# Kernel optimization log

Measured on AMD Instinct MI355X. Metric: run time of the kernel, lower is better.

The kernel has to match this reference:

```python
import jax, jax.numpy as jnp
import numpy as np
import math

B, N, D = 2, 4096, 1024
H, R, M = 16, 4, 8
BUCKET = 64

def setup_inputs() -> dict:
    key = jax.random.key(0)
    k1, k2, k3, k4, k5 = jax.random.split(key, 5)
    d = D // H
    return {
        "query": jax.random.normal(k1, (B, N, D), jnp.float32),
        "key": jax.random.normal(k2, (B, N, D), jnp.float32),
        "value": jax.random.normal(k3, (B, N, D), jnp.float32),
        "valence": jax.random.uniform(k4, (B,), jnp.float32),
        "hash_projections": jax.random.normal(k5, (R, H, d, M), jnp.float32),
        "valence_scale": jnp.ones((1,), jnp.float32),
    }

def reference(query, key, value, valence, hash_projections, valence_scale):
    b, n, dm = query.shape
    h = H
    d = dm // h
    r, _, _, m = hash_projections.shape
    c = n // BUCKET  # n_buckets (must divide exactly, matching torch view)
    # (B,N,D) -> (B,H,N,d)
    Q = query.reshape(b, n, h, d).transpose(0, 2, 1, 3)
    K = key.reshape(b, n, h, d).transpose(0, 2, 1, 3)
    V = value.reshape(b, n, h, d).transpose(0, 2, 1, 3)
    # LSH hash: argmax over M random projections per round -> (B,R,H,N)
    hashes = jnp.einsum('bhnd,rhdm->brhnm', Q, hash_projections)
    codes = jnp.argmax(hashes, axis=-1)
    # valence modulation (torch: scale.long().clamp(1, M); int truncation)
    scale = 1.0 + valence_scale[0] * valence.mean()
    scale_i = jnp.clip(scale.astype(jnp.int32), 1, m)
    codes = codes * scale_i
    # sort positions by hash code per (B,R,H)
    idx = jnp.argsort(codes, axis=-1)  # (B,R,H,N)
    idx_e = idx[..., None]  # (B,R,H,N,1), broadcasts over d
    K_sorted = jnp.take_along_axis(K[:, None], idx_e, axis=3)  # (B,R,H,N,d)
    V_sorted = jnp.take_along_axis(V[:, None], idx_e, axis=3)
    Kb = K_sorted.reshape(b, r, h, c, BUCKET, d)
    Vb = V_sorted.reshape(b, r, h, c, BUCKET, d)
    # NOTE: queries are bucketed in ORIGINAL order (faithful to source)
    Qb = Q.reshape(b, h, c, BUCKET, d)
    scores = jnp.einsum('bhcsd,brhced->brhcse', Qb, Kb) / math.sqrt(d)
    attn = jax.nn.softmax(scores, axis=-1)  # (B,R,H,C,S,E)
    outb = jnp.einsum('brhcse,brhced->brhcsd', attn, Vb)
    out = outb.reshape(b, r, h, n, d).mean(axis=1)  # average over hash rounds
    out = out.transpose(0, 2, 1, 3).reshape(b, n, dm)  # dropout is identity (eval)
    return out, attn.mean(axis=(1, 2))
```

## Files before the change

kernel.cpp:

```cpp
#include <hip/hip_runtime.h>
#include <hip/hip_bf16.h>

#define BB 2
#define NN 4096
#define DD 1024
#define HH 16
#define RR 4
#define MM 8
#define CC 64
#define DH 64
#define PAD 68

typedef __attribute__((ext_vector_type(8))) short bf16x8;
typedef __attribute__((ext_vector_type(4))) float f32x4;
typedef unsigned long long u64;

__device__ __forceinline__ unsigned short f2bf(float x) {
  union { __hip_bfloat16 b; unsigned short u; } cv;
  cv.b = __float2bfloat16(x);
  return cv.u;
}
__device__ __forceinline__ int swz(int row, int colbyte) {
  return row * 128 + (colbyte ^ ((row & 7) << 4));
}
__device__ __forceinline__ bf16x8 pack8(float4 a, float4 b, float sc) {
  bf16x8 r;
  const float* pa = (const float*)&a;
  const float* pb = (const float*)&b;
#pragma unroll
  for (int j = 0; j < 4; ++j) {
    r[j] = (short)f2bf(pa[j] * sc);
    r[j + 4] = (short)f2bf(pb[j] * sc);
  }
  return r;
}
__device__ __forceinline__ void load_lds16(const void* g, void* l) {
  __builtin_amdgcn_global_load_lds(
      (const __attribute__((address_space(1))) unsigned*)g,
      (__attribute__((address_space(3))) unsigned*)l, 16, 0, 0);
}

__global__ __launch_bounds__(256) void k_hash(const float* __restrict__ q,
                                              const float* __restrict__ proj,
                                              int* __restrict__ codes) {
  int blk = blockIdx.x;
  int nc = blk & (CC - 1);
  int h = (blk >> 6) & (HH - 1);
  int b = blk >> 10;
  __shared__ float Qs[64][PAD];
  __shared__ float Ps[DH][MM];
  __shared__ float Ss[64][9];
  int tid = threadIdx.x;
  const float* qbase = q + ((size_t)(b * NN + nc * 64) * DD + h * DH);
  for (int f = tid; f < 1024; f += 256) {
    int row = f >> 4, c4 = f & 15;
    *(float4*)&Qs[row][c4 * 4] = *(const float4*)(qbase + (size_t)row * DD + c4 * 4);
  }
  int nl = tid >> 3, m = tid & 7;
  for (int r = 0; r < RR; ++r) {
    const float* pbase = proj + (size_t)(r * HH + h) * DH * MM;
    for (int f = tid; f < DH * MM / 4; f += 256)
      ((float4*)Ps)[f] = ((const float4*)pbase)[f];
    __syncthreads();
    float s0 = 0.f, s1 = 0.f;
#pragma unroll
    for (int kk = 0; kk < DH; ++kk) {
      float p = Ps[kk][m];
      s0 += Qs[nl][kk] * p;
      s1 += Qs[nl + 32][kk] * p;
    }
    Ss[nl][m] = s0;
    Ss[nl + 32][m] = s1;
    __syncthreads();
    if (tid < 64) {
      float best = Ss[tid][0];
      int bm = 0;
#pragma unroll
      for (int mm = 1; mm < MM; ++mm) {
        float vv = Ss[tid][mm];
        if (vv > best) { best = vv; bm = mm; }
      }
      codes[(size_t)((b * RR + r) * HH + h) * NN + nc * 64 + tid] = bm;
    }
    __syncthreads();
  }
}

__global__ __launch_bounds__(256) void k_sort(const int* __restrict__ codes,
                                              int* __restrict__ idxo) {
  int gblk = blockIdx.x;
  const int* cg = codes + (size_t)gblk * NN;
  int* ig = idxo + (size_t)gblk * NN;
  int tid = threadIdx.x, lane = tid & 63, w = tid >> 6;
  __shared__ u64 wtot[4][2];
  int myc[16];
#pragma unroll
  for (int qd = 0; qd < 4; ++qd) {
    int4 t4 = ((const int4*)(cg + tid * 16))[qd];
    myc[qd * 4 + 0] = t4.x; myc[qd * 4 + 1] = t4.y;
    myc[qd * 4 + 2] = t4.z; myc[qd * 4 + 3] = t4.w;
  }
  u64 c01 = 0, c23 = 0;
#pragma unroll
  for (int i = 0; i < 16; ++i) {
    int k = myc[i];
    u64 one = 1ull << (16 * (k & 3));
    if (k < 4) c01 += one; else c23 += one;
  }
  u64 i01 = c01, i23 = c23;
#pragma unroll
  for (int d = 1; d < 64; d <<= 1) {
    u64 t0 = __shfl_up(i01, d);
    u64 t1 = __shfl_up(i23, d);
    if (lane >= d) { i01 += t0; i23 += t1; }
  }
  if (lane == 63) { wtot[w][0] = i01; wtot[w][1] = i23; }
  __syncthreads();
  u64 base01 = 0, base23 = 0, g01 = 0, g23 = 0;
#pragma unroll
  for (int ww = 0; ww < 4; ++ww) {
    u64 a = wtot[ww][0], bq = wtot[ww][1];
    if (ww < w) { base01 += a; base23 += bq; }
    g01 += a; g23 += bq;
  }
  u64 p01 = g01 + (g01 << 16); p01 += (p01 << 32);
  u64 p23 = g23 + (g23 << 16); p23 += (p23 << 32);
  u64 cb01 = p01 << 16;
  u64 tot01 = (p01 >> 48) & 0xffffull;
  u64 cb23 = (p23 << 16) + tot01 * 0x0001000100010001ull;
  u64 o01 = cb01 + base01 + (i01 - c01);
  u64 o23 = cb23 + base23 + (i23 - c23);
#pragma unroll
  for (int i = 0; i < 16; ++i) {
    int k = myc[i];
    int sh = 16 * (k & 3);
    int off;
    if (k < 4) { off = (int)((o01 >> sh) & 0xffffull); o01 += 1ull << sh; }
    else       { off = (int)((o23 >> sh) & 0xffffull); o23 += 1ull << sh; }
    ig[off] = tid * 16 + i;
  }
}

__global__ __launch_bounds__(256, 4) void k_attn(const float* __restrict__ q,
                                                 const float* __restrict__ kmat,
                                                 const float* __restrict__ vmat,
                                                 const int* __restrict__ idxs,
                                                 float* __restrict__ out,
                                                 float* __restrict__ attn_part,
                                                 float* __restrict__ attn_out,
                                                 int atomic_attn) {
  __shared__ __align__(16) char KL[16384];
  __shared__ __align__(16) char VTl[8192];
  __shared__ __align__(16) char Plds[8192];
  __shared__ int sidx[RR][64];

  int blk = ((int)blockIdx.x & 7) * 256 + ((int)blockIdx.x >> 3);
  int cblk = blk & 63;
  int h = (blk >> 6) & 15;
  int b = blk >> 10;
  int tid = threadIdx.x;
  int lane = tid & 63;
  int w = tid >> 6;
  int g = lane >> 4;
  int cl = lane & 15;
  int cl2 = lane & 15, sub = lane >> 4;
  int e2 = tid & 31, dg = tid >> 5;

  sidx[tid >> 6][tid & 63] =
      idxs[(size_t)((b * RR + (tid >> 6)) * HH + h) * NN + cblk * 64 + (tid & 63)];
  __syncthreads();

  const char* kbase = (const char*)(kmat + (size_t)b * NN * DD + h * DH);
  const float* vbase = vmat + (size_t)b * NN * DD + h * DH;

  const float* qrow = q + (size_t)(b * NN + cblk * 64 + 16 * w + cl) * DD + h * DH;
  bf16x8 qh[2];
#pragma unroll
  for (int ks = 0; ks < 2; ++ks)
    qh[ks] = pack8(*(const float4*)(qrow + 32 * ks + 8 * g),
                   *(const float4*)(qrow + 32 * ks + 8 * g + 4), 0.125f);

  f32x4 acc_o[4];
  float attA[4][4];
#pragma unroll
  for (int t = 0; t < 4; ++t) {
    acc_o[t] = (f32x4){0.f, 0.f, 0.f, 0.f};
#pragma unroll
    for (int i = 0; i < 4; ++i) attA[t][i] = 0.f;
  }

  float4 vtmp[4];
  {
    int row = sidx[0][16 * w + cl2];
    const char* gsrc = kbase + (size_t)row * 4096 + sub * 16;
#pragma unroll
    for (int qq = 0; qq < 4; ++qq)
      load_lds16(gsrc + qq * 64, KL + w * 4096 + qq * 1024);
  }
  {
    const float* v0 = vbase + (size_t)sidx[0][2 * e2] * DD + 8 * dg;
    const float* v1 = vbase + (size_t)sidx[0][2 * e2 + 1] * DD + 8 * dg;
    vtmp[0] = *(const float4*)v0; vtmp[1] = *(const float4*)(v0 + 4);
    vtmp[2] = *(const float4*)v1; vtmp[3] = *(const float4*)(v1 + 4);
    const float* r0 = (const float*)&vtmp[0];
    const float* r1 = (const float*)&vtmp[2];
#pragma unroll
    for (int j = 0; j < 8; ++j) {
      unsigned pk = (unsigned)f2bf(r0[j]) | ((unsigned)f2bf(r1[j]) << 16);
      *(unsigned*)(VTl + swz(8 * dg + j, 4 * e2)) = pk;
    }
  }

#pragma unroll
  for (int r = 0; r < RR; ++r) {
    __syncthreads();

    if (r < 3) {
      const float* v0 = vbase + (size_t)sidx[r + 1][2 * e2] * DD + 8 * dg;
      const float* v1 = vbase + (size_t)sidx[r + 1][2 * e2 + 1] * DD + 8 * dg;
      vtmp[0] = *(const float4*)v0; vtmp[1] = *(const float4*)(v0 + 4);
      vtmp[2] = *(const float4*)v1; vtmp[3] = *(const float4*)(v1 + 4);
    }

    f32x4 s4[4];
#pragma unroll
    for (int t = 0; t < 4; ++t) s4[t] = (f32x4){0.f, 0.f, 0.f, 0.f};
    __builtin_amdgcn_s_setprio(1);
#pragma unroll
    for (int t = 0; t < 4; ++t) {
#pragma unroll
      for (int ks = 0; ks < 2; ++ks) {
        int base = t * 4096 + (2 * ks + (g >> 1)) * 1024 + (g & 1) * 512 + cl * 16;
        f32x4 f0 = *(const f32x4*)(KL + base);
        f32x4 f1 = *(const f32x4*)(KL + base + 256);
        const unsigned* u0 = (const unsigned*)&f0;
        const unsigned* u1 = (const unsigned*)&f1;
        union { bf16x8 v; unsigned u[4]; } kb;
        kb.u[0] = __builtin_amdgcn_perm(u0[1], u0[0], 0x07060302);
        kb.u[1] = __builtin_amdgcn_perm(u0[3], u0[2], 0x07060302);
        kb.u[2] = __builtin_amdgcn_perm(u1[1], u1[0], 0x07060302);
        kb.u[3] = __builtin_amdgcn_perm(u1[3], u1[2], 0x07060302);
        s4[t] = __builtin_amdgcn_mfma_f32_16x16x32_bf16(qh[ks], kb.v, s4[t], 0, 0, 0);
      }
    }
    __builtin_amdgcn_s_setprio(0);

#pragma unroll
    for (int i = 0; i < 4; ++i) {
      float mx = fmaxf(fmaxf(s4[0][i], s4[1][i]), fmaxf(s4[2][i], s4[3][i]));
      mx = fmaxf(mx, __shfl_xor(mx, 1));
      mx = fmaxf(mx, __shfl_xor(mx, 2));
      mx = fmaxf(mx, __shfl_xor(mx, 4));
      mx = fmaxf(mx, __shfl_xor(mx, 8));
      float sm = 0.f;
#pragma unroll
      for (int t = 0; t < 4; ++t) {
        float e = __expf(s4[t][i] - mx);
        s4[t][i] = e;
        sm += e;
      }
      sm += __shfl_xor(sm, 1);
      sm += __shfl_xor(sm, 2);
      sm += __shfl_xor(sm, 4);
      sm += __shfl_xor(sm, 8);
      float inv = __builtin_amdgcn_rcpf(sm);
#pragma unroll
      for (int t = 0; t < 4; ++t) {
        s4[t][i] *= inv;
        attA[t][i] += s4[t][i];
      }
    }
#pragma unroll
    for (int i = 0; i < 4; ++i) {
      int srow = 16 * w + 4 * g + i;
#pragma unroll
      for (int t = 0; t < 4; ++t)
        *(unsigned short*)(Plds + swz(srow, 2 * (16 * t + cl))) = f2bf(s4[t][i]);
    }
    bf16x8 pa[2];
#pragma unroll
    for (int ks = 0; ks < 2; ++ks)
      pa[ks] = *(const bf16x8*)(Plds + swz(16 * w + cl, ks * 64 + g * 16));
    __builtin_amdgcn_s_setprio(1);
#pragma unroll
    for (int t = 0; t < 4; ++t)
#pragma unroll
      for (int ks = 0; ks < 2; ++ks) {
        bf16x8 vt = *(const bf16x8*)(VTl + swz(16 * t + cl, ks * 64 + g * 16));
        acc_o[t] = __builtin_amdgcn_mfma_f32_16x16x32_bf16(pa[ks], vt, acc_o[t], 0, 0, 0);
      }
    __builtin_amdgcn_s_setprio(0);

    __syncthreads();

    if (r < 3) {
      int row = sidx[r + 1][16 * w + cl2];
      const char* gsrc = kbase + (size_t)row * 4096 + sub * 16;
#pragma unroll
      for (int qq = 0; qq < 4; ++qq)
        load_lds16(gsrc + qq * 64, KL + w * 4096 + qq * 1024);
      const float* r0 = (const float*)&vtmp[0];
      const float* r1 = (const float*)&vtmp[2];
#pragma unroll
      for (int j = 0; j < 8; ++j) {
        unsigned pk = (unsigned)f2bf(r0[j]) | ((unsigned)f2bf(r1[j]) << 16);
        *(unsigned*)(VTl + swz(8 * dg + j, 4 * e2)) = pk;
      }
    }
  }

#pragma unroll
  for (int i = 0; i < 4; ++i) {
    int srow = 16 * w + 4 * g + i;
    size_t obase = (size_t)(b * NN + cblk * 64 + srow) * DD + h * DH;
#pragma unroll
    for (int t = 0; t < 4; ++t)
      out[obase + 16 * t + cl] = acc_o[t][i] * 0.25f;
  }
  if (atomic_attn) {
    const float sc = 1.f / (RR * HH);
#pragma unroll
    for (int i = 0; i < 4; ++i) {
      int srow = 16 * w + 4 * g + i;
#pragma unroll
      for (int t = 0; t < 4; ++t)
        atomicAdd(attn_out + (((size_t)b * CC + cblk) * 64 + srow) * 64 + 16 * t + cl,
                  attA[t][i] * sc);
    }
  } else {
#pragma unroll
    for (int i = 0; i < 4; ++i) {
      int srow = 16 * w + 4 * g + i;
#pragma unroll
      for (int t = 0; t < 4; ++t)
        attn_part[(((size_t)(b * HH + h) * CC + cblk) * 64 + srow) * 64 + 16 * t + cl] =
            attA[t][i];
    }
  }
}

__global__ __launch_bounds__(256) void k_attn_reduce(const float* __restrict__ part,
                                                     float* __restrict__ attn_out) {
  size_t o = (size_t)blockIdx.x * 256 + threadIdx.x;
  int se = (int)(o & 4095);
  size_t bc = o >> 12;
  int c = (int)(bc & (CC - 1));
  int b = (int)(bc >> 6);
  float s = 0.f;
  const float* p = part + ((size_t)b * HH * CC + c) * 4096 + se;
#pragma unroll
  for (int h = 0; h < HH; ++h) s += p[(size_t)h * CC * 4096];
  attn_out[o] = s * (1.f / (RR * HH));
}

extern "C" void kernel_launch(void* const* d_in, const int* in_sizes, int n_in,
                              void* d_out, int out_size, void* d_ws, size_t ws_size,
                              hipStream_t stream) {
  const float* q = (const float*)d_in[0];
  const float* k = (const float*)d_in[1];
  const float* v = (const float*)d_in[2];
  const float* proj = (const float*)d_in[4];
  float* out = (float*)d_out;
  float* attn_out = out + (size_t)BB * NN * DD;

  int* codes = (int*)d_ws;
  int* idxs = codes + (size_t)BB * RR * HH * NN;
  float* attn_part = (float*)(idxs + (size_t)BB * RR * HH * NN);
  size_t need = (size_t)BB * RR * HH * NN * 8 + (size_t)BB * HH * CC * 4096 * 4;
  int atomic_attn = (ws_size < need) ? 1 : 0;
  if (atomic_attn)
    hipMemsetAsync(attn_out, 0, (size_t)BB * CC * 4096 * sizeof(float), stream);

  k_hash<<<BB * HH * CC, 256, 0, stream>>>(q, proj, codes);
  k_sort<<<BB * RR * HH, 256, 0, stream>>>(codes, idxs);
  k_attn<<<BB * HH * CC, 256, 0, stream>>>(q, k, v, idxs, out, attn_part, attn_out, atomic_attn);
  if (!atomic_attn)
    k_attn_reduce<<<BB * CC * 4096 / 256, 256, 0, stream>>>(attn_part, attn_out);
}
```

Baseline: 88.82 us.

## Process four query chunks per block with double-buffered K/V LDS pipeline

Each attention block now handles four 64-row chunks instead of one, so the grid shrinks from 2048 to 512 blocks. K and V tiles get double-buffered LDS so the next round's (or next chunk's) gather overlaps the current MFMA work, and there is one barrier per round instead of two. The next chunk's Q rows are prefetched mid-loop. In exchange the block uses more LDS, occupancy is set to 2 blocks per CU, and 512 blocks may underfill the 256-CU device with less latency hiding.

```diff
diff --git a/kernel.cpp b/kernel.cpp
--- a/kernel.cpp
+++ b/kernel.cpp
@@ -9,6 +9,7 @@
 #define MM 8
 #define CC 64
 #define DH 64
+#define CG 4
 #define PAD 68
 
 typedef __attribute__((ext_vector_type(8))) short bf16x8;
@@ -141,7 +142,42 @@
   }
 }
 
-__global__ __launch_bounds__(256, 4) void k_attn(const float* __restrict__ q,
+__device__ __forceinline__ void write_c(const f32x4* acc_o, const float attA[4][4],
+                                        int b, int h, int cblk, int w, int g, int cl,
+                                        float* __restrict__ out,
+                                        float* __restrict__ attn_part,
+                                        float* __restrict__ attn_out, int atomic_attn) {
+#pragma unroll
+  for (int i = 0; i < 4; ++i) {
+    int srow = 16 * w + 4 * g + i;
+    size_t obase = (size_t)(b * NN + cblk * 64 + srow) * DD + h * DH;
+#pragma unroll
+    for (int t = 0; t < 4; ++t)
+      out[obase + 16 * t + cl] = acc_o[t][i] * 0.25f;
+  }
+  if (atomic_attn) {
+    const float sc = 1.f / (RR * HH);
+#pragma unroll
+    for (int i = 0; i < 4; ++i) {
+      int srow = 16 * w + 4 * g + i;
+#pragma unroll
+      for (int t = 0; t < 4; ++t)
+        atomicAdd(attn_out + (((size_t)b * CC + cblk) * 64 + srow) * 64 + 16 * t + cl,
+                  attA[t][i] * sc);
+    }
+  } else {
+#pragma unroll
+    for (int i = 0; i < 4; ++i) {
+      int srow = 16 * w + 4 * g + i;
+#pragma unroll
+      for (int t = 0; t < 4; ++t)
+        attn_part[(((size_t)(b * HH + h) * CC + cblk) * 64 + srow) * 64 + 16 * t + cl] =
+            attA[t][i];
+    }
+  }
+}
+
+__global__ __launch_bounds__(256, 2) void k_attn(const float* __restrict__ q,
                                                  const float* __restrict__ kmat,
                                                  const float* __restrict__ vmat,
                                                  const int* __restrict__ idxs,
@@ -149,15 +185,18 @@
                                                  float* __restrict__ attn_part,
                                                  float* __restrict__ attn_out,
                                                  int atomic_attn) {
-  __shared__ __align__(16) char KL[16384];
-  __shared__ __align__(16) char VTl[8192];
+  __shared__ __align__(16) char KL[2][16384];
+  __shared__ __align__(16) char VTl[2][8192];
   __shared__ __align__(16) char Plds[8192];
-  __shared__ int sidx[RR][64];
-
-  int blk = ((int)blockIdx.x & 7) * 256 + ((int)blockIdx.x >> 3);
-  int cblk = blk & 63;
-  int h = (blk >> 6) & 15;
-  int b = blk >> 10;
+  __shared__ int sidxL[RR][CG * 64];
+
+  int bid = blockIdx.x;
+  int blk = (bid & 7) * 64 + (bid >> 3);
+  int cgi = blk & 15;
+  int h = (blk >> 4) & 15;
+  int b = blk >> 8;
+  int cbase = cgi * CG;
+
   int tid = threadIdx.x;
   int lane = tid & 63;
   int w = tid >> 6;
@@ -166,19 +205,48 @@
   int cl2 = lane & 15, sub = lane >> 4;
   int e2 = tid & 31, dg = tid >> 5;
 
-  sidx[tid >> 6][tid & 63] =
-      idxs[(size_t)((b * RR + (tid >> 6)) * HH + h) * NN + cblk * 64 + (tid & 63)];
-  __syncthreads();
+#pragma unroll
+  for (int k = 0; k < RR; ++k)
+    sidxL[k][tid] = idxs[(size_t)((b * RR + k) * HH + h) * NN + cbase * 64 + tid];
 
   const char* kbase = (const char*)(kmat + (size_t)b * NN * DD + h * DH);
   const float* vbase = vmat + (size_t)b * NN * DD + h * DH;
-
-  const float* qrow = q + (size_t)(b * NN + cblk * 64 + 16 * w + cl) * DD + h * DH;
+  const float* qrow0 = q + (size_t)(b * NN + cbase * 64 + 16 * w + cl) * DD + h * DH;
+
+  float4 qraw[4];
+#pragma unroll
+  for (int ks = 0; ks < 2; ++ks) {
+    qraw[2 * ks] = *(const float4*)(qrow0 + 32 * ks + 8 * g);
+    qraw[2 * ks + 1] = *(const float4*)(qrow0 + 32 * ks + 8 * g + 4);
+  }
+  __syncthreads();
+
+  {
+    const int* s0 = &sidxL[0][0];
+    const float* v0 = vbase + (size_t)s0[2 * e2] * DD + 8 * dg;
+    const float* v1 = vbase + (size_t)s0[2 * e2 + 1] * DD + 8 * dg;
+    float4 vt4[4];
+    vt4[0] = *(const float4*)v0; vt4[1] = *(const float4*)(v0 + 4);
+    vt4[2] = *(const float4*)v1; vt4[3] = *(const float4*)(v1 + 4);
+    int row = s0[16 * w + cl2];
+    const char* gsrc = kbase + (size_t)row * 4096 + sub * 16;
+#pragma unroll
+    for (int qq = 0; qq < 4; ++qq)
+      load_lds16(gsrc + qq * 64, KL[0] + w * 4096 + qq * 1024);
+    const float* r0 = (const float*)&vt4[0];
+    const float* r1 = (const float*)&vt4[2];
+#pragma unroll
+    for (int j = 0; j < 8; ++j) {
+      unsigned pk = (unsigned)f2bf(r0[j]) | ((unsigned)f2bf(r1[j]) << 16);
+      *(unsigned*)(VTl[0] + swz(8 * dg + j, 4 * e2)) = pk;
+    }
+  }
+  __syncthreads();
+
   bf16x8 qh[2];
 #pragma unroll
   for (int ks = 0; ks < 2; ++ks)
-    qh[ks] = pack8(*(const float4*)(qrow + 32 * ks + 8 * g),
-                   *(const float4*)(qrow + 32 * ks + 8 * g + 4), 0.125f);
+    qh[ks] = pack8(qraw[2 * ks], qraw[2 * ks + 1], 0.125f);
 
   f32x4 acc_o[4];
   float attA[4][4];
@@ -189,152 +257,132 @@
     for (int i = 0; i < 4; ++i) attA[t][i] = 0.f;
   }
 
-  float4 vtmp[4];
-  {
-    int row = sidx[0][16 * w + cl2];
-    const char* gsrc = kbase + (size_t)row * 4096 + sub * 16;
-#pragma unroll
-    for (int qq = 0; qq < 4; ++qq)
-      load_lds16(gsrc + qq * 64, KL + w * 4096 + qq * 1024);
-  }
-  {
-    const float* v0 = vbase + (size_t)sidx[0][2 * e2] * DD + 8 * dg;
-    const float* v1 = vbase + (size_t)sidx[0][2 * e2 + 1] * DD + 8 * dg;
-    vtmp[0] = *(const float4*)v0; vtmp[1] = *(const float4*)(v0 + 4);
-    vtmp[2] = *(const float4*)v1; vtmp[3] = *(const float4*)(v1 + 4);
-    const float* r0 = (const float*)&vtmp[0];
-    const float* r1 = (const float*)&vtmp[2];
-#pragma unroll
-    for (int j = 0; j < 8; ++j) {
-      unsigned pk = (unsigned)f2bf(r0[j]) | ((unsigned)f2bf(r1[j]) << 16);
-      *(unsigned*)(VTl + swz(8 * dg + j, 4 * e2)) = pk;
-    }
-  }
-
-#pragma unroll
-  for (int r = 0; r < RR; ++r) {
-    __syncthreads();
-
-    if (r < 3) {
-      const float* v0 = vbase + (size_t)sidx[r + 1][2 * e2] * DD + 8 * dg;
-      const float* v1 = vbase + (size_t)sidx[r + 1][2 * e2 + 1] * DD + 8 * dg;
-      vtmp[0] = *(const float4*)v0; vtmp[1] = *(const float4*)(v0 + 4);
-      vtmp[2] = *(const float4*)v1; vtmp[3] = *(const float4*)(v1 + 4);
-    }
-
-    f32x4 s4[4];
-#pragma unroll
-    for (int t = 0; t < 4; ++t) s4[t] = (f32x4){0.f, 0.f, 0.f, 0.f};
-    __builtin_amdgcn_s_setprio(1);
-#pragma unroll
-    for (int t = 0; t < 4; ++t) {
-#pragma unroll
-      for (int ks = 0; ks < 2; ++ks) {
-        int base = t * 4096 + (2 * ks + (g >> 1)) * 1024 + (g & 1) * 512 + cl * 16;
-        f32x4 f0 = *(const f32x4*)(KL + base);
-        f32x4 f1 = *(const f32x4*)(KL + base + 256);
-        const unsigned* u0 = (const unsigned*)&f0;
-        const unsigned* u1 = (const unsigned*)&f1;
-        union { bf16x8 v; unsigned u[4]; } kb;
-        kb.u[0] = __builtin_amdgcn_perm(u0[1], u0[0], 0x07060302);
-        kb.u[1] = __builtin_amdgcn_perm(u0[3], u0[2], 0x07060302);
-        kb.u[2] = __builtin_amdgcn_perm(u1[1], u1[0], 0x07060302);
-        kb.u[3] = __builtin_amdgcn_perm(u1[3], u1[2], 0x07060302);
-        s4[t] = __builtin_amdgcn_mfma_f32_16x16x32_bf16(qh[ks], kb.v, s4[t], 0, 0, 0);
-      }
-    }
-    __builtin_amdgcn_s_setprio(0);
-
-#pragma unroll
-    for (int i = 0; i < 4; ++i) {
-      float mx = fmaxf(fmaxf(s4[0][i], s4[1][i]), fmaxf(s4[2][i], s4[3][i]));
-      mx = fmaxf(mx, __shfl_xor(mx, 1));
-      mx = fmaxf(mx, __shfl_xor(mx, 2));
-      mx = fmaxf(mx, __shfl_xor(mx, 4));
-      mx = fmaxf(mx, __shfl_xor(mx, 8));
-      float sm = 0.f;
+#pragma unroll 1
+  for (int cq = 0; cq < CG; ++cq) {
+#pragma unroll
+    for (int r = 0; r < RR; ++r) {
+      const char* KLcur = KL[r & 1];
+      const char* VTcur = VTl[r & 1];
+      const bool has_next = (r < RR - 1) || (cq < CG - 1);
+
+      float4 vt4[4];
+      if (has_next) {
+        const int* sn = (r < RR - 1) ? &sidxL[r + 1][cq * 64]
+                                     : &sidxL[0][(cq + 1) * 64];
+        const float* v0 = vbase + (size_t)sn[2 * e2] * DD + 8 * dg;
+        const float* v1 = vbase + (size_t)sn[2 * e2 + 1] * DD + 8 * dg;
+        vt4[0] = *(const float4*)v0; vt4[1] = *(const float4*)(v0 + 4);
+        vt4[2] = *(const float4*)v1; vt4[3] = *(const float4*)(v1 + 4);
+        int row = sn[16 * w + cl2];
+        const char* gsrc = kbase + (size_t)row * 4096 + sub * 16;
+#pragma unroll
+        for (int qq = 0; qq < 4; ++qq)
+          load_lds16(gsrc + qq * 64, KL[(r + 1) & 1] + w * 4096 + qq * 1024);
+      }
+      if (r == 1 && cq < CG - 1) {
+        const float* qrn = qrow0 + (size_t)(cq + 1) * 64 * DD;
+#pragma unroll
+        for (int ks = 0; ks < 2; ++ks) {
+          qraw[2 * ks] = *(const float4*)(qrn + 32 * ks + 8 * g);
+          qraw[2 * ks + 1] = *(const float4*)(qrn + 32 * ks + 8 * g + 4);
+        }
+      }
+
+      f32x4 s4[4];
+#pragma unroll
+      for (int t = 0; t < 4; ++t) s4[t] = (f32x4){0.f, 0.f, 0.f, 0.f};
+      __builtin_amdgcn_s_setprio(1);
 #pragma unroll
       for (int t = 0; t < 4; ++t) {
-        float e = __expf(s4[t][i] - mx);
-        s4[t][i] = e;
-        sm += e;
-      }
-      sm += __shfl_xor(sm, 1);
-      sm += __shfl_xor(sm, 2);
-      sm += __shfl_xor(sm, 4);
-      sm += __shfl_xor(sm, 8);
-      float inv = __builtin_amdgcn_rcpf(sm);
+#pragma unroll
+        for (int ks = 0; ks < 2; ++ks) {
+          int base = t * 4096 + (2 * ks + (g >> 1)) * 1024 + (g & 1) * 512 + cl * 16;
+          f32x4 f0 = *(const f32x4*)(KLcur + base);
+          f32x4 f1 = *(const f32x4*)(KLcur + base + 256);
+          const unsigned* u0 = (const unsigned*)&f0;
+          const unsigned* u1 = (const unsigned*)&f1;
+          union { bf16x8 v; unsigned u[4]; } kb;
+          kb.u[0] = __builtin_amdgcn_perm(u0[1], u0[0], 0x07060302);
+          kb.u[1] = __builtin_amdgcn_perm(u0[3], u0[2], 0x07060302);
+          kb.u[2] = __builtin_amdgcn_perm(u1[1], u1[0], 0x07060302);
+          kb.u[3] = __builtin_amdgcn_perm(u1[3], u1[2], 0x07060302);
+          s4[t] = __builtin_amdgcn_mfma_f32_16x16x32_bf16(qh[ks], kb.v, s4[t], 0, 0, 0);
+        }
+      }
+      __builtin_amdgcn_s_setprio(0);
+
+#pragma unroll
+      for (int i = 0; i < 4; ++i) {
+        float mx = fmaxf(fmaxf(s4[0][i], s4[1][i]), fmaxf(s4[2][i], s4[3][i]));
+        mx = fmaxf(mx, __shfl_xor(mx, 1));
+        mx = fmaxf(mx, __shfl_xor(mx, 2));
+        mx = fmaxf(mx, __shfl_xor(mx, 4));
+        mx = fmaxf(mx, __shfl_xor(mx, 8));
+        float sm = 0.f;
+#pragma unroll
+        for (int t = 0; t < 4; ++t) {
+          float e = __expf(s4[t][i] - mx);
+          s4[t][i] = e;
+          sm += e;
+        }
+        sm += __shfl_xor(sm, 1);
+        sm += __shfl_xor(sm, 2);
+        sm += __shfl_xor(sm, 4);
+        sm += __shfl_xor(sm, 8);
+        float inv = __builtin_amdgcn_rcpf(sm);
+#pragma unroll
+        for (int t = 0; t < 4; ++t) {
+          s4[t][i] *= inv;
+          attA[t][i] += s4[t][i];
+        }
+      }
+
+#pragma unroll
+      for (int i = 0; i < 4; ++i) {
+        int srow = 16 * w + 4 * g + i;
+#pragma unroll
+        for (int t = 0; t < 4; ++t)
+          *(unsigned short*)(Plds + swz(srow, 2 * (16 * t + cl))) = f2bf(s4[t][i]);
+      }
+      bf16x8 pa[2];
+#pragma unroll
+      for (int ks = 0; ks < 2; ++ks)
+        pa[ks] = *(const bf16x8*)(Plds + swz(16 * w + cl, ks * 64 + g * 16));
+
+      __builtin_amdgcn_s_setprio(1);
+#pragma unroll
+      for (int t = 0; t < 4; ++t)
+#pragma unroll
+        for (int ks = 0; ks < 2; ++ks) {
+          bf16x8 vt = *(const bf16x8*)(VTcur + swz(16 * t + cl, ks * 64 + g * 16));
+          acc_o[t] = __builtin_amdgcn_mfma_f32_16x16x32_bf16(pa[ks], vt, acc_o[t], 0, 0, 0);
+        }
+      __builtin_amdgcn_s_setprio(0);
+
+      if (has_next) {
+        const float* r0 = (const float*)&vt4[0];
+        const float* r1 = (const float*)&vt4[2];
+#pragma unroll
+        for (int j = 0; j < 8; ++j) {
+          unsigned pk = (unsigned)f2bf(r0[j]) | ((unsigned)f2bf(r1[j]) << 16);
+          *(unsigned*)(VTl[(r + 1) & 1] + swz(8 * dg + j, 4 * e2)) = pk;
+        }
+        __syncthreads();
+      }
+    }
+
+    write_c(acc_o, attA, b, h, cbase + cq, w, g, cl, out, attn_part, attn_out,
+            atomic_attn);
+    if (cq < CG - 1) {
 #pragma unroll
       for (int t = 0; t < 4; ++t) {
-        s4[t][i] *= inv;
-        attA[t][i] += s4[t][i];
-      }
-    }
-#pragma unroll
-    for (int i = 0; i < 4; ++i) {
-      int srow = 16 * w + 4 * g + i;
-#pragma unroll
-      for (int t = 0; t < 4; ++t)
-        *(unsigned short*)(Plds + swz(srow, 2 * (16 * t + cl))) = f2bf(s4[t][i]);
-    }
-    bf16x8 pa[2];
-#pragma unroll
-    for (int ks = 0; ks < 2; ++ks)
-      pa[ks] = *(const bf16x8*)(Plds + swz(16 * w + cl, ks * 64 + g * 16));
-    __builtin_amdgcn_s_setprio(1);
-#pragma unroll
-    for (int t = 0; t < 4; ++t)
-#pragma unroll
-      for (int ks = 0; ks < 2; ++ks) {
-        bf16x8 vt = *(const bf16x8*)(VTl + swz(16 * t + cl, ks * 64 + g * 16));
-        acc_o[t] = __builtin_amdgcn_mfma_f32_16x16x32_bf16(pa[ks], vt, acc_o[t], 0, 0, 0);
-      }
-    __builtin_amdgcn_s_setprio(0);
-
-    __syncthreads();
-
-    if (r < 3) {
-      int row = sidx[r + 1][16 * w + cl2];
-      const char* gsrc = kbase + (size_t)row * 4096 + sub * 16;
-#pragma unroll
-      for (int qq = 0; qq < 4; ++qq)
-        load_lds16(gsrc + qq * 64, KL + w * 4096 + qq * 1024);
-      const float* r0 = (const float*)&vtmp[0];
-      const float* r1 = (const float*)&vtmp[2];
-#pragma unroll
-      for (int j = 0; j < 8; ++j) {
-        unsigned pk = (unsigned)f2bf(r0[j]) | ((unsigned)f2bf(r1[j]) << 16);
-        *(unsigned*)(VTl + swz(8 * dg + j, 4 * e2)) = pk;
-      }
-    }
-  }
-
-#pragma unroll
-  for (int i = 0; i < 4; ++i) {
-    int srow = 16 * w + 4 * g + i;
-    size_t obase = (size_t)(b * NN + cblk * 64 + srow) * DD + h * DH;
-#pragma unroll
-    for (int t = 0; t < 4; ++t)
-      out[obase + 16 * t + cl] = acc_o[t][i] * 0.25f;
-  }
-  if (atomic_attn) {
-    const float sc = 1.f / (RR * HH);
-#pragma unroll
-    for (int i = 0; i < 4; ++i) {
-      int srow = 16 * w + 4 * g + i;
-#pragma unroll
-      for (int t = 0; t < 4; ++t)
-        atomicAdd(attn_out + (((size_t)b * CC + cblk) * 64 + srow) * 64 + 16 * t + cl,
-                  attA[t][i] * sc);
-    }
-  } else {
-#pragma unroll
-    for (int i = 0; i < 4; ++i) {
-      int srow = 16 * w + 4 * g + i;
-#pragma unroll
-      for (int t = 0; t < 4; ++t)
-        attn_part[(((size_t)(b * HH + h) * CC + cblk) * 64 + srow) * 64 + 16 * t + cl] =
-            attA[t][i];
+        acc_o[t] = (f32x4){0.f, 0.f, 0.f, 0.f};
+#pragma unroll
+        for (int i = 0; i < 4; ++i) attA[t][i] = 0.f;
+      }
+#pragma unroll
+      for (int ks = 0; ks < 2; ++ks)
+        qh[ks] = pack8(qraw[2 * ks], qraw[2 * ks + 1], 0.125f);
     }
   }
 }
@@ -373,7 +421,8 @@
 
   k_hash<<<BB * HH * CC, 256, 0, stream>>>(q, proj, codes);
   k_sort<<<BB * RR * HH, 256, 0, stream>>>(codes, idxs);
-  k_attn<<<BB * HH * CC, 256, 0, stream>>>(q, k, v, idxs, out, attn_part, attn_out, atomic_attn);
+  k_attn<<<BB * HH * (CC / CG), 256, 0, stream>>>(q, k, v, idxs, out, attn_part,
+                                                  attn_out, atomic_attn);
   if (!atomic_attn)
     k_attn_reduce<<<BB * CC * 4096 / 256, 256, 0, stream>>>(attn_part, attn_out);
 }
```

Result: slower. 98.72 us (+11.1%).

## Pre-convert K/V to per-head bf16 panels and double-buffer K tiles in attention

Applied to the files above, without the earlier changes.

Adds a pre-pass kernel that converts K and V from fp32 to bf16 and lays them out per (batch, head) as contiguous 128-byte rows. The attention kernel then gathers half as many bytes per sorted row and skips per-round conversion. It also double-buffers the K LDS tile, swaps the MFMA operand order so the softmax reduction needs fewer cross-lane shuffles, and vectorises the output stores. The cost is an extra full pass over K and V plus additional workspace, and the fallback switches to atomics when the workspace is too small.

```diff
diff --git a/kernel.cpp b/kernel.cpp
--- a/kernel.cpp
+++ b/kernel.cpp
@@ -12,6 +12,7 @@
 #define PAD 68
 
 typedef __attribute__((ext_vector_type(8))) short bf16x8;
+typedef __attribute__((ext_vector_type(8))) unsigned short ushort8;
 typedef __attribute__((ext_vector_type(4))) float f32x4;
 typedef unsigned long long u64;
 
@@ -38,6 +39,33 @@
   __builtin_amdgcn_global_load_lds(
       (const __attribute__((address_space(1))) unsigned*)g,
       (__attribute__((address_space(3))) unsigned*)l, 16, 0, 0);
+}
+
+__global__ __launch_bounds__(256) void k_cvt(const float* __restrict__ kmat,
+                                             const float* __restrict__ vmat,
+                                             unsigned short* __restrict__ kbf,
+                                             unsigned short* __restrict__ vbf) {
+  int bid = blockIdx.x;
+  int b = bid >> 8;
+  int n0 = (bid & 255) * 16;
+  int tid = threadIdx.x;
+  int h = tid >> 4, d4 = tid & 15;
+#pragma unroll 4
+  for (int it = 0; it < 16; ++it) {
+    int row = n0 + it;
+    size_t src = (size_t)(b * NN + row) * DD + tid * 4;
+    float4 kv = *(const float4*)(kmat + src);
+    float4 vv = *(const float4*)(vmat + src);
+    size_t dst = ((size_t)(b * HH + h) * NN + row) * 64 + d4 * 4;
+    const float* kf = (const float*)&kv;
+    const float* vf = (const float*)&vv;
+    u64 kp = (u64)f2bf(kf[0]) | ((u64)f2bf(kf[1]) << 16) |
+             ((u64)f2bf(kf[2]) << 32) | ((u64)f2bf(kf[3]) << 48);
+    u64 vp = (u64)f2bf(vf[0]) | ((u64)f2bf(vf[1]) << 16) |
+             ((u64)f2bf(vf[2]) << 32) | ((u64)f2bf(vf[3]) << 48);
+    *(u64*)(kbf + dst) = kp;
+    *(u64*)(vbf + dst) = vp;
+  }
 }
 
 __global__ __launch_bounds__(256) void k_hash(const float* __restrict__ q,
@@ -142,19 +170,20 @@
 }
 
 __global__ __launch_bounds__(256, 4) void k_attn(const float* __restrict__ q,
-                                                 const float* __restrict__ kmat,
-                                                 const float* __restrict__ vmat,
+                                                 const unsigned short* __restrict__ kbf,
+                                                 const unsigned short* __restrict__ vbf,
                                                  const int* __restrict__ idxs,
                                                  float* __restrict__ out,
                                                  float* __restrict__ attn_part,
                                                  float* __restrict__ attn_out,
                                                  int atomic_attn) {
-  __shared__ __align__(16) char KL[16384];
-  __shared__ __align__(16) char VTl[8192];
-  __shared__ __align__(16) char Plds[8192];
+  __shared__ __align__(16) char KB[2][8192];
+  __shared__ __align__(16) char VT[8192];
+  __shared__ __align__(16) char PL[8192];
   __shared__ int sidx[RR][64];
 
-  int blk = ((int)blockIdx.x & 7) * 256 + ((int)blockIdx.x >> 3);
+  int bid = blockIdx.x;
+  int blk = (bid & 7) * 256 + (bid >> 3);
   int cblk = blk & 63;
   int h = (blk >> 6) & 15;
   int b = blk >> 10;
@@ -163,15 +192,13 @@
   int w = tid >> 6;
   int g = lane >> 4;
   int cl = lane & 15;
-  int cl2 = lane & 15, sub = lane >> 4;
-  int e2 = tid & 31, dg = tid >> 5;
+  int e2 = tid & 31, dg = (tid >> 5) & 7;
 
   sidx[tid >> 6][tid & 63] =
       idxs[(size_t)((b * RR + (tid >> 6)) * HH + h) * NN + cblk * 64 + (tid & 63)];
-  __syncthreads();
-
-  const char* kbase = (const char*)(kmat + (size_t)b * NN * DD + h * DH);
-  const float* vbase = vmat + (size_t)b * NN * DD + h * DH;
+
+  const char* kp = (const char*)(kbf + (size_t)(b * HH + h) * NN * 64);
+  const unsigned short* vp = vbf + (size_t)(b * HH + h) * NN * 64;
 
   const float* qrow = q + (size_t)(b * NN + cblk * 64 + 16 * w + cl) * DD + h * DH;
   bf16x8 qh[2];
@@ -180,6 +207,24 @@
     qh[ks] = pack8(*(const float4*)(qrow + 32 * ks + 8 * g),
                    *(const float4*)(qrow + 32 * ks + 8 * g + 4), 0.125f);
 
+  __syncthreads();
+
+  {
+    int row = sidx[0][16 * w + cl];
+    const char* gs = kp + (size_t)row * 128 + g * 16;
+    load_lds16(gs, KB[0] + w * 2048);
+    load_lds16(gs + 64, KB[0] + w * 2048 + 1024);
+    ushort8 v0r = *(const ushort8*)(vp + (size_t)sidx[0][2 * e2] * 64 + dg * 8);
+    ushort8 v1r = *(const ushort8*)(vp + (size_t)sidx[0][2 * e2 + 1] * 64 + dg * 8);
+#pragma unroll
+    for (int j = 0; j < 8; ++j) {
+      unsigned pk = (unsigned)(unsigned short)v0r[j] |
+                    ((unsigned)(unsigned short)v1r[j] << 16);
+      *(unsigned*)(VT + swz(8 * dg + j, 4 * e2)) = pk;
+    }
+  }
+  __syncthreads();
+
   f32x4 acc_o[4];
   float attA[4][4];
 #pragma unroll
@@ -189,37 +234,16 @@
     for (int i = 0; i < 4; ++i) attA[t][i] = 0.f;
   }
 
-  float4 vtmp[4];
-  {
-    int row = sidx[0][16 * w + cl2];
-    const char* gsrc = kbase + (size_t)row * 4096 + sub * 16;
-#pragma unroll
-    for (int qq = 0; qq < 4; ++qq)
-      load_lds16(gsrc + qq * 64, KL + w * 4096 + qq * 1024);
-  }
-  {
-    const float* v0 = vbase + (size_t)sidx[0][2 * e2] * DD + 8 * dg;
-    const float* v1 = vbase + (size_t)sidx[0][2 * e2 + 1] * DD + 8 * dg;
-    vtmp[0] = *(const float4*)v0; vtmp[1] = *(const float4*)(v0 + 4);
-    vtmp[2] = *(const float4*)v1; vtmp[3] = *(const float4*)(v1 + 4);
-    const float* r0 = (const float*)&vtmp[0];
-    const float* r1 = (const float*)&vtmp[2];
-#pragma unroll
-    for (int j = 0; j < 8; ++j) {
-      unsigned pk = (unsigned)f2bf(r0[j]) | ((unsigned)f2bf(r1[j]) << 16);
-      *(unsigned*)(VTl + swz(8 * dg + j, 4 * e2)) = pk;
-    }
-  }
-
 #pragma unroll
   for (int r = 0; r < RR; ++r) {
-    __syncthreads();
-
-    if (r < 3) {
-      const float* v0 = vbase + (size_t)sidx[r + 1][2 * e2] * DD + 8 * dg;
-      const float* v1 = vbase + (size_t)sidx[r + 1][2 * e2 + 1] * DD + 8 * dg;
-      vtmp[0] = *(const float4*)v0; vtmp[1] = *(const float4*)(v0 + 4);
-      vtmp[2] = *(const float4*)v1; vtmp[3] = *(const float4*)(v1 + 4);
+    ushort8 n0r, n1r;
+    if (r < RR - 1) {
+      int row = sidx[r + 1][16 * w + cl];
+      const char* gs = kp + (size_t)row * 128 + g * 16;
+      load_lds16(gs, KB[(r + 1) & 1] + w * 2048);
+      load_lds16(gs + 64, KB[(r + 1) & 1] + w * 2048 + 1024);
+      n0r = *(const ushort8*)(vp + (size_t)sidx[r + 1][2 * e2] * 64 + dg * 8);
+      n1r = *(const ushort8*)(vp + (size_t)sidx[r + 1][2 * e2 + 1] * 64 + dg * 8);
     }
 
     f32x4 s4[4];
@@ -227,114 +251,99 @@
     for (int t = 0; t < 4; ++t) s4[t] = (f32x4){0.f, 0.f, 0.f, 0.f};
     __builtin_amdgcn_s_setprio(1);
 #pragma unroll
-    for (int t = 0; t < 4; ++t) {
+    for (int t = 0; t < 4; ++t)
 #pragma unroll
       for (int ks = 0; ks < 2; ++ks) {
-        int base = t * 4096 + (2 * ks + (g >> 1)) * 1024 + (g & 1) * 512 + cl * 16;
-        f32x4 f0 = *(const f32x4*)(KL + base);
-        f32x4 f1 = *(const f32x4*)(KL + base + 256);
-        const unsigned* u0 = (const unsigned*)&f0;
-        const unsigned* u1 = (const unsigned*)&f1;
-        union { bf16x8 v; unsigned u[4]; } kb;
-        kb.u[0] = __builtin_amdgcn_perm(u0[1], u0[0], 0x07060302);
-        kb.u[1] = __builtin_amdgcn_perm(u0[3], u0[2], 0x07060302);
-        kb.u[2] = __builtin_amdgcn_perm(u1[1], u1[0], 0x07060302);
-        kb.u[3] = __builtin_amdgcn_perm(u1[3], u1[2], 0x07060302);
-        s4[t] = __builtin_amdgcn_mfma_f32_16x16x32_bf16(qh[ks], kb.v, s4[t], 0, 0, 0);
-      }
-    }
-    __builtin_amdgcn_s_setprio(0);
-
-#pragma unroll
-    for (int i = 0; i < 4; ++i) {
-      float mx = fmaxf(fmaxf(s4[0][i], s4[1][i]), fmaxf(s4[2][i], s4[3][i]));
-      mx = fmaxf(mx, __shfl_xor(mx, 1));
-      mx = fmaxf(mx, __shfl_xor(mx, 2));
-      mx = fmaxf(mx, __shfl_xor(mx, 4));
-      mx = fmaxf(mx, __shfl_xor(mx, 8));
-      float sm = 0.f;
-#pragma unroll
-      for (int t = 0; t < 4; ++t) {
-        float e = __expf(s4[t][i] - mx);
-        s4[t][i] = e;
-        sm += e;
-      }
-      sm += __shfl_xor(sm, 1);
-      sm += __shfl_xor(sm, 2);
-      sm += __shfl_xor(sm, 4);
-      sm += __shfl_xor(sm, 8);
-      float inv = __builtin_amdgcn_rcpf(sm);
-#pragma unroll
-      for (int t = 0; t < 4; ++t) {
-        s4[t][i] *= inv;
-        attA[t][i] += s4[t][i];
-      }
-    }
-#pragma unroll
-    for (int i = 0; i < 4; ++i) {
-      int srow = 16 * w + 4 * g + i;
-#pragma unroll
-      for (int t = 0; t < 4; ++t)
-        *(unsigned short*)(Plds + swz(srow, 2 * (16 * t + cl))) = f2bf(s4[t][i]);
-    }
-    bf16x8 pa[2];
-#pragma unroll
-    for (int ks = 0; ks < 2; ++ks)
-      pa[ks] = *(const bf16x8*)(Plds + swz(16 * w + cl, ks * 64 + g * 16));
-    __builtin_amdgcn_s_setprio(1);
-#pragma unroll
-    for (int t = 0; t < 4; ++t)
-#pragma unroll
-      for (int ks = 0; ks < 2; ++ks) {
-        bf16x8 vt = *(const bf16x8*)(VTl + swz(16 * t + cl, ks * 64 + g * 16));
-        acc_o[t] = __builtin_amdgcn_mfma_f32_16x16x32_bf16(pa[ks], vt, acc_o[t], 0, 0, 0);
+        bf16x8 kf = *(const bf16x8*)(KB[r & 1] + t * 2048 + ks * 1024 + g * 256 + cl * 16);
+        s4[t] = __builtin_amdgcn_mfma_f32_16x16x32_bf16(kf, qh[ks], s4[t], 0, 0, 0);
       }
     __builtin_amdgcn_s_setprio(0);
 
-    __syncthreads();
-
-    if (r < 3) {
-      int row = sidx[r + 1][16 * w + cl2];
-      const char* gsrc = kbase + (size_t)row * 4096 + sub * 16;
-#pragma unroll
-      for (int qq = 0; qq < 4; ++qq)
-        load_lds16(gsrc + qq * 64, KL + w * 4096 + qq * 1024);
-      const float* r0 = (const float*)&vtmp[0];
-      const float* r1 = (const float*)&vtmp[2];
+    {
+      f32x4 m4 = s4[0];
+#pragma unroll
+      for (int t = 1; t < 4; ++t)
+#pragma unroll
+        for (int i = 0; i < 4; ++i) m4[i] = fmaxf(m4[i], s4[t][i]);
+      float mx = fmaxf(fmaxf(m4[0], m4[1]), fmaxf(m4[2], m4[3]));
+      mx = fmaxf(mx, __shfl_xor(mx, 16));
+      mx = fmaxf(mx, __shfl_xor(mx, 32));
+      float sm = 0.f;
+#pragma unroll
+      for (int t = 0; t < 4; ++t)
+#pragma unroll
+        for (int i = 0; i < 4; ++i) {
+          float e = __expf(s4[t][i] - mx);
+          s4[t][i] = e;
+          sm += e;
+        }
+      sm += __shfl_xor(sm, 16);
+      sm += __shfl_xor(sm, 32);
+      float inv = __builtin_amdgcn_rcpf(sm);
+#pragma unroll
+      for (int t = 0; t < 4; ++t)
+#pragma unroll
+        for (int i = 0; i < 4; ++i) {
+          s4[t][i] *= inv;
+          attA[t][i] += s4[t][i];
+        }
+    }
+
+#pragma unroll
+    for (int t = 0; t < 4; ++t) {
+      u64 pk = (u64)f2bf(s4[t][0]) | ((u64)f2bf(s4[t][1]) << 16) |
+               ((u64)f2bf(s4[t][2]) << 32) | ((u64)f2bf(s4[t][3]) << 48);
+      *(u64*)(PL + w * 2048 + swz(cl, 32 * t + 8 * g)) = pk;
+    }
+    bf16x8 pa[2];
+#pragma unroll
+    for (int ks = 0; ks < 2; ++ks)
+      pa[ks] = *(const bf16x8*)(PL + w * 2048 + swz(cl, 64 * ks + 16 * g));
+
+    __builtin_amdgcn_s_setprio(1);
+#pragma unroll
+    for (int t = 0; t < 4; ++t)
+#pragma unroll
+      for (int ks = 0; ks < 2; ++ks) {
+        bf16x8 vt = *(const bf16x8*)(VT + swz(16 * t + cl, ks * 64 + g * 16));
+        acc_o[t] = __builtin_amdgcn_mfma_f32_16x16x32_bf16(vt, pa[ks], acc_o[t], 0, 0, 0);
+      }
+    __builtin_amdgcn_s_setprio(0);
+
+    if (r < RR - 1) {
+      __syncthreads();
 #pragma unroll
       for (int j = 0; j < 8; ++j) {
-        unsigned pk = (unsigned)f2bf(r0[j]) | ((unsigned)f2bf(r1[j]) << 16);
-        *(unsigned*)(VTl + swz(8 * dg + j, 4 * e2)) = pk;
+        unsigned pk = (unsigned)(unsigned short)n0r[j] |
+                      ((unsigned)(unsigned short)n1r[j] << 16);
+        *(unsigned*)(VT + swz(8 * dg + j, 4 * e2)) = pk;
       }
-    }
-  }
-
-#pragma unroll
-  for (int i = 0; i < 4; ++i) {
-    int srow = 16 * w + 4 * g + i;
-    size_t obase = (size_t)(b * NN + cblk * 64 + srow) * DD + h * DH;
-#pragma unroll
-    for (int t = 0; t < 4; ++t)
-      out[obase + 16 * t + cl] = acc_o[t][i] * 0.25f;
-  }
+      __syncthreads();
+    }
+  }
+
+  int srow = 16 * w + cl;
+  size_t ob = (size_t)(b * NN + cblk * 64 + srow) * DD + h * DH + 4 * g;
+#pragma unroll
+  for (int t = 0; t < 4; ++t) {
+    float4 o = make_float4(acc_o[t][0] * 0.25f, acc_o[t][1] * 0.25f,
+                           acc_o[t][2] * 0.25f, acc_o[t][3] * 0.25f);
+    *(float4*)(out + ob + 16 * t) = o;
+  }
+  size_t ab = (((size_t)(b * HH + h) * CC + cblk) * 64 + srow) * 64 + 4 * g;
   if (atomic_attn) {
     const float sc = 1.f / (RR * HH);
-#pragma unroll
-    for (int i = 0; i < 4; ++i) {
-      int srow = 16 * w + 4 * g + i;
-#pragma unroll
-      for (int t = 0; t < 4; ++t)
-        atomicAdd(attn_out + (((size_t)b * CC + cblk) * 64 + srow) * 64 + 16 * t + cl,
-                  attA[t][i] * sc);
-    }
+    size_t abase = (((size_t)b * CC + cblk) * 64 + srow) * 64 + 4 * g;
+#pragma unroll
+    for (int t = 0; t < 4; ++t)
+#pragma unroll
+      for (int i = 0; i < 4; ++i)
+        atomicAdd(attn_out + abase + 16 * t + i, attA[t][i] * sc);
   } else {
 #pragma unroll
-    for (int i = 0; i < 4; ++i) {
-      int srow = 16 * w + 4 * g + i;
-#pragma unroll
-      for (int t = 0; t < 4; ++t)
-        attn_part[(((size_t)(b * HH + h) * CC + cblk) * 64 + srow) * 64 + 16 * t + cl] =
-            attA[t][i];
+    for (int t = 0; t < 4; ++t) {
+      float4 o = make_float4(attA[t][0], attA[t][1], attA[t][2], attA[t][3]);
+      *(float4*)(attn_part + ab + 16 * t) = o;
     }
   }
 }
@@ -363,17 +372,26 @@
   float* out = (float*)d_out;
   float* attn_out = out + (size_t)BB * NN * DD;
 
+  const size_t n_codes = (size_t)BB * RR * HH * NN;
+  const size_t n_panel = (size_t)BB * HH * NN * 64;
+  const size_t n_part  = (size_t)BB * HH * CC * 4096;
+
   int* codes = (int*)d_ws;
-  int* idxs = codes + (size_t)BB * RR * HH * NN;
-  float* attn_part = (float*)(idxs + (size_t)BB * RR * HH * NN);
-  size_t need = (size_t)BB * RR * HH * NN * 8 + (size_t)BB * HH * CC * 4096 * 4;
-  int atomic_attn = (ws_size < need) ? 1 : 0;
+  int* idxs = codes + n_codes;
+  unsigned short* kbf = (unsigned short*)(idxs + n_codes);
+  unsigned short* vbf = kbf + n_panel;
+  float* attn_part = (float*)(vbf + n_panel);
+
+  size_t need_full = n_codes * 8 + n_panel * 4 + n_part * 4;
+  int atomic_attn = (ws_size < need_full) ? 1 : 0;
   if (atomic_attn)
     hipMemsetAsync(attn_out, 0, (size_t)BB * CC * 4096 * sizeof(float), stream);
 
+  k_cvt<<<BB * (NN / 16), 256, 0, stream>>>(k, v, kbf, vbf);
   k_hash<<<BB * HH * CC, 256, 0, stream>>>(q, proj, codes);
   k_sort<<<BB * RR * HH, 256, 0, stream>>>(codes, idxs);
-  k_attn<<<BB * HH * CC, 256, 0, stream>>>(q, k, v, idxs, out, attn_part, attn_out, atomic_attn);
+  k_attn<<<BB * HH * CC, 256, 0, stream>>>(q, kbf, vbf, idxs, out, attn_part,
+                                           attn_out, atomic_attn);
   if (!atomic_attn)
     k_attn_reduce<<<BB * CC * 4096 / 256, 256, 0, stream>>>(attn_part, attn_out);
 }
```

New measurement: 90.70 us. 1.02x slower.
